# Kernel tuning notes

Hardware: AMD Instinct MI355X
Metric: run time of the kernel (lower is better)

The kernel has to match this reference:

```python
import jax, jax.numpy as jnp
import numpy as np

EPS = 1e-6


def setup_inputs() -> dict:
    key = jax.random.key(0)
    ks = jax.random.split(key, 7)
    T, B, D, n, r = 512, 32, 1024, 1024, 8
    x = jax.random.normal(ks[0], (T, B, D), dtype=jnp.float32)
    # xavier_uniform-like init for weights
    def xavier(k, shape):
        fan_in, fan_out = shape[1], shape[0]
        a = float(np.sqrt(6.0 / (fan_in + fan_out)))
        return jax.random.uniform(k, shape, dtype=jnp.float32, minval=-a, maxval=a)
    W_k = xavier(ks[1], (n, D))
    W_v = xavier(ks[2], (n, D))
    W_q = xavier(ks[3], (n, D))
    W_kr = xavier(ks[4], (r, n))
    U0 = jnp.zeros((B, n, r), dtype=jnp.float32)
    V0 = jax.random.normal(ks[5], (B, n, r), dtype=jnp.float32) * 0.01
    return {"x": x, "W_k": W_k, "W_v": W_v, "W_q": W_q, "W_kr": W_kr, "U0": U0, "V0": V0}


def reference(x, W_k, W_v, W_q, W_kr, U0, V0):
    # x: [T, B, D]; state S = U @ V^T with U,V: [B, n, r]
    k = jnp.einsum('tbd,nd->tbn', x, W_k)
    v = jnp.einsum('tbd,nd->tbn', x, W_v)
    q = jnp.einsum('tbd,nd->tbn', x, W_q)
    V = V0  # V is never updated in the recurrence

    def step(U, kvq):
        k_t, v_t, q_t = kvq  # each [B, n]
        k_norm = k_t / (jnp.linalg.norm(k_t, axis=-1, keepdims=True) + EPS)
        Vtk = jnp.einsum('bnr,bn->br', V, k_norm)
        retrieved = jnp.einsum('bnr,br->bn', U, Vtk)
        delta = v_t - retrieved
        k_r = k_norm @ W_kr.T  # [B, r]
        U_new = jnp.tanh(U + delta[:, :, None] * k_r[:, None, :])
        Vtq = jnp.einsum('bnr,bn->br', V, q_t)
        Sq = jnp.einsum('bnr,br->bn', U_new, Vtq)
        out = Sq * jax.nn.silu(Sq)
        return U_new, out

    U_final, output = jax.lax.scan(step, U0, (k, v, q))
    return output, (U_final, V)
```

## Files before the change

### kernel.cpp

```cpp
#include <hip/hip_runtime.h>
#include <hip/hip_bf16.h>

typedef __attribute__((ext_vector_type(8))) short short8;
typedef __attribute__((ext_vector_type(4))) short short4v;
typedef __attribute__((ext_vector_type(4))) float f32x4;
typedef unsigned short u16;

__device__ inline float b2f(u16 u) {
    unsigned int i = ((unsigned int)u) << 16;
    float f; __builtin_memcpy(&f, &i, 4); return f;
}
__device__ inline u16 f2b(float f) {
    unsigned int i; __builtin_memcpy(&i, &f, 4);
    unsigned int r = (i + 0x7FFFu + ((i >> 16) & 1u)) >> 16;
    return (u16)r;
}

__device__ inline float xsum32(float x) {
    unsigned u; __builtin_memcpy(&u, &x, 4);
    auto r = __builtin_amdgcn_permlane32_swap(u, u, false, false);
    unsigned s0 = r[0], s1 = r[1];
    float f0, f1; __builtin_memcpy(&f0, &s0, 4); __builtin_memcpy(&f1, &s1, 4);
    return f0 + f1;
}

#define GLDS(g, l) __builtin_amdgcn_global_load_lds( \
    (const __attribute__((address_space(1))) void*)(g), \
    (__attribute__((address_space(3))) void*)(l), 16, 0, 0)

#define KWAIT(N) asm volatile("s_waitcnt lgkmcnt(0)\n\t" \
                              "s_waitcnt vmcnt(" #N ")\n\t" \
                              "s_barrier" ::: "memory")

__global__ __launch_bounds__(256) void cvt_k(const float* __restrict__ src,
                                             u16* __restrict__ dst, int n4)
{
    const int i = blockIdx.x * blockDim.x + threadIdx.x;
    if (i < n4) {
        const f32x4 v = ((const f32x4*)src)[i];
        short4v o;
        o.x = (short)f2b(v.x); o.y = (short)f2b(v.y);
        o.z = (short)f2b(v.z); o.w = (short)f2b(v.w);
        ((short4v*)dst)[i] = o;
    }
}

__global__ __launch_bounds__(256) void vT_k(const float* __restrict__ V0,
                                            float* __restrict__ V0T)
{
    const int gid = blockIdx.x * 256 + threadIdx.x;
    const int b = gid >> 9, j = (gid >> 6) & 7, n0 = (gid & 63) * 16;
    const float* src = V0 + (long)b * 8192 + (long)n0 * 8 + j;
    float* dst = V0T + (long)b * 8192 + (long)j * 1024 + n0;
#pragma unroll
    for (int i = 0; i < 16; i += 4) {
        f32x4 o = { src[(i + 0) * 8], src[(i + 1) * 8],
                    src[(i + 2) * 8], src[(i + 3) * 8] };
        *(f32x4*)(dst + i) = o;
    }
}

__global__ __launch_bounds__(512) void gemm256_kvq(
    const u16* __restrict__ Xbf, const u16* __restrict__ Wbf,
    u16* __restrict__ Ko, u16* __restrict__ Vo, u16* __restrict__ Qo)
{
    __shared__ u16 lds[65536];

    const int bid = blockIdx.x;
    const int swz = (bid & 7) * 96 + (bid >> 3);
    const int bm = swz / 12, bnx = swz % 12;
    const int widx = bnx >> 2;
    const int nbase = (bnx & 3) * 256;
    const int m0 = bm * 256;
    const u16* Wp = Wbf + (long)widx * 1048576;
    u16* O = (widx == 0) ? Ko : (widx == 1 ? Vo : Qo);

    const int tid = threadIdx.x;
    const int w = tid >> 6;
    const int lane = tid & 63;
    const int wm = (w >> 2) * 128;
    const int wn = (w & 3) * 64;
    const int ln = lane & 15, qd = lane >> 4;

    const int q8 = lane >> 3, s8 = lane & 7;
    const int cc = s8 ^ q8;
    const u16* p0; const u16* p1; const u16* p2; const u16* p3;
    {
        auto mk = [&](int l) -> const u16* {
            const int r = l * 64 + w * 8 + q8;
            return (cc < 4)
                ? (Xbf + (long)(m0 + r) * 1024 + cc * 8)
                : (Wp  + (long)(nbase + r) * 1024 + (cc - 4) * 8);
        };
        p0 = mk(0); p1 = mk(1); p2 = mk(2); p3 = mk(3);
    }

    int aoff[8], boff[4];
#pragma unroll
    for (int mf = 0; mf < 8; ++mf) {
        const int ro = wm + mf * 16 + ln;
        aoff[mf] = ro * 128 + ((qd ^ (ro & 7)) * 16);
    }
#pragma unroll
    for (int nf = 0; nf < 4; ++nf) {
        const int rb = wn + nf * 16 + ln;
        boff[nf] = rb * 128 + (((4 + qd) ^ (rb & 7)) * 16);
    }

    f32x4 acc[8][4];
#pragma unroll
    for (int i = 0; i < 8; ++i)
#pragma unroll
        for (int j = 0; j < 4; ++j) acc[i][j] = (f32x4){0.f, 0.f, 0.f, 0.f};

#pragma unroll
    for (int tt = 0; tt < 3; ++tt) {
        char* db = (char*)lds + tt * 32768 + w * 1024;
        GLDS(p0, db);
        GLDS(p1, db + 8192);
        GLDS(p2, db + 16384);
        GLDS(p3, db + 24576);
        p0 += 32; p1 += 32; p2 += 32; p3 += 32;
    }
    KWAIT(8);

    for (int t = 0; t < 32; ++t) {
        const char* bb = (const char*)lds + (t & 3) * 32768;
        short8 a[8], bfr[4];
#pragma unroll
        for (int mf = 0; mf < 4; ++mf) a[mf] = *(const short8*)(bb + aoff[mf]);
#pragma unroll
        for (int nf = 0; nf < 4; ++nf) bfr[nf] = *(const short8*)(bb + boff[nf]);
        if (t < 29) {
            char* db = (char*)lds + ((t + 3) & 3) * 32768 + w * 1024;
            GLDS(p0, db);
            GLDS(p1, db + 8192);
            p0 += 32; p1 += 32;
        }
        __builtin_amdgcn_s_setprio(1);
#pragma unroll
        for (int mf = 0; mf < 4; ++mf)
#pragma unroll
            for (int nf = 0; nf < 4; ++nf)
                acc[mf][nf] = __builtin_amdgcn_mfma_f32_16x16x32_bf16(
                    a[mf], bfr[nf], acc[mf][nf], 0, 0, 0);
        __builtin_amdgcn_s_setprio(0);
#pragma unroll
        for (int mf = 4; mf < 8; ++mf) a[mf] = *(const short8*)(bb + aoff[mf]);
        if (t < 29) {
            char* db = (char*)lds + ((t + 3) & 3) * 32768 + w * 1024;
            GLDS(p2, db + 16384);
            GLDS(p3, db + 24576);
            p2 += 32; p3 += 32;
        }
        __builtin_amdgcn_s_setprio(1);
#pragma unroll
        for (int mf = 4; mf < 8; ++mf)
#pragma unroll
            for (int nf = 0; nf < 4; ++nf)
                acc[mf][nf] = __builtin_amdgcn_mfma_f32_16x16x32_bf16(
                    a[mf], bfr[nf], acc[mf][nf], 0, 0, 0);
        __builtin_amdgcn_s_setprio(0);
        if (t < 29)       KWAIT(8);
        else if (t == 29) KWAIT(4);
        else if (t == 30) KWAIT(0);
    }

#pragma unroll
    for (int mf = 0; mf < 8; ++mf) {
#pragma unroll
        for (int nf = 0; nf < 4; ++nf) {
            const int r0 = m0 + wm + mf * 16 + qd * 4;
            const int c  = nbase + wn + nf * 16 + ln;
#pragma unroll
            for (int r = 0; r < 4; ++r)
                O[(long)(r0 + r) * 1024 + c] = f2b(acc[mf][nf][r]);
        }
    }
}

__global__ __launch_bounds__(256) void scal_k(
    const u16* __restrict__ K, const u16* __restrict__ Q,
    const float* __restrict__ V0T, const float* __restrict__ Wkr,
    float* __restrict__ S)
{
    const int b  = blockIdx.x & 31;
    const int t0 = (blockIdx.x >> 5) * 4;
    const int tid = threadIdx.x;
    const int j = tid & 7, c = tid >> 3;
    const int n0 = c * 32;

    f32x4 vv[8], ww[8];
    {
        const f32x4* vp = (const f32x4*)(V0T + (long)b * 8192 + (long)j * 1024 + n0);
        const f32x4* wp = (const f32x4*)(Wkr + (long)j * 1024 + n0);
#pragma unroll
        for (int i = 0; i < 8; i++) { vv[i] = vp[i]; ww[i] = wp[i]; }
    }

    float avk[4], akr[4], avq[4], ass[4];
#pragma unroll
    for (int dt = 0; dt < 4; dt++) { avk[dt] = akr[dt] = avq[dt] = ass[dt] = 0.f; }

#pragma unroll
    for (int dt = 0; dt < 4; dt++) {
        const long m = (long)(t0 + dt) * 32 + b;
        const short8* kp = (const short8*)(K + m * 1024 + n0);
        const short8* qp = (const short8*)(Q + m * 1024 + n0);
#pragma unroll
        for (int i = 0; i < 4; i++) {
            const short8 kb = kp[i], qb = qp[i];
#pragma unroll
            for (int e = 0; e < 8; e++) {
                const int idx = i * 8 + e;
                const float kv = b2f((u16)kb[e]);
                const float qv = b2f((u16)qb[e]);
                const float vj = vv[idx >> 2][idx & 3];
                const float wj = ww[idx >> 2][idx & 3];
                avk[dt] = fmaf(vj, kv, avk[dt]);
                akr[dt] = fmaf(wj, kv, akr[dt]);
                avq[dt] = fmaf(vj, qv, avq[dt]);
                ass[dt] = fmaf(kv, kv, ass[dt]);
            }
        }
    }

    __shared__ float red[4][4][3][8];
    __shared__ float ssr[4][4];
    const int wave = tid >> 6, lane = tid & 63;
#pragma unroll
    for (int dt = 0; dt < 4; dt++) {
        float a = avk[dt], k2 = akr[dt], q = avq[dt], s = ass[dt];
#pragma unroll
        for (int off = 8; off < 64; off <<= 1) {
            a  += __shfl_xor(a,  off, 64);
            k2 += __shfl_xor(k2, off, 64);
            q  += __shfl_xor(q,  off, 64);
            s  += __shfl_xor(s,  off, 64);
        }
        if (lane < 8) {
            red[wave][dt][0][lane] = a;
            red[wave][dt][1][lane] = k2;
            red[wave][dt][2][lane] = q;
        }
        if (lane == 0) ssr[wave][dt] = s;
    }
    __syncthreads();
    if (tid < 128) {
        const int dt = tid >> 5, rr = tid & 31;
        if (rr < 24) {
            const int v = rr >> 3, jj = rr & 7;
            float s = red[0][dt][v][jj] + red[1][dt][v][jj] +
                      red[2][dt][v][jj] + red[3][dt][v][jj];
            if (v != 2) {
                const float n2 = ssr[0][dt] + ssr[1][dt] + ssr[2][dt] + ssr[3][dt];
                const float inv = 1.0f / (sqrtf(n2) + 1e-6f);
                s *= (v == 0) ? (0.5f * inv) : (2.0f * inv);
            } else {
                s *= 0.5f;
            }
            S[((long)b * 512 + t0 + dt) * 32 + v * 8 + jj] = s;
        }
    }
}

__global__ __launch_bounds__(128) void scan_k(
    const u16* __restrict__ Vbuf, const float* __restrict__ S,
    const float* __restrict__ U0, float* __restrict__ outp,
    float* __restrict__ Ufin)
{
    __shared__ float Sl[512 * 32];

    const int b = blockIdx.x >> 4;
    const int chunk = blockIdx.x & 15;
    const int wave = threadIdx.x >> 6, lane = threadIdx.x & 63;
    const int rh = lane >> 5;
    const int n = chunk * 64 + wave * 32 + (lane & 31);
    const int so = rh * 4;

    {
        const f32x4* Sg = (const f32x4*)(S + (long)b * 16384);
        f32x4* Sd = (f32x4*)Sl;
        for (int i = threadIdx.x; i < 4096; i += 128) Sd[i] = Sg[i];
    }

    float U[4];
    {
        const float* u0 = U0 + ((long)b * 1024 + n) * 8 + so;
#pragma unroll
        for (int j2 = 0; j2 < 4; j2++) U[j2] = 2.0f * u0[j2];
    }

    const u16* vp0 = Vbuf + (long)b * 1024 + n;
    u16 vnx[16];
#pragma unroll
    for (int i = 0; i < 16; i++) vnx[i] = vp0[(long)i * 32768];

    __syncthreads();

    f32x4 sc[3], sn[3];
#pragma unroll
    for (int r = 0; r < 3; r++) sc[r] = *(const f32x4*)&Sl[r * 8 + so];
#pragma unroll
    for (int r = 0; r < 3; r++) sn[r] = *(const f32x4*)&Sl[32 + r * 8 + so];

    float* op = outp + (long)b * 1024 + n;

    for (int t0 = 0; t0 < 512; t0 += 16) {
        float vcur[16];
#pragma unroll
        for (int i = 0; i < 16; i++) vcur[i] = b2f(vnx[i]);
        const int tn = (t0 + 16 < 512) ? (t0 + 16) : t0;
#pragma unroll
        for (int i = 0; i < 16; i++) vnx[i] = vp0[(long)(tn + i) * 32768];

#pragma unroll
        for (int i = 0; i < 16; i++) {
            const int t = t0 + i;
            const int tf = (t + 2 < 512) ? (t + 2) : t;
            f32x4 sm[3];
#pragma unroll
            for (int r = 0; r < 3; r++) sm[r] = *(const f32x4*)&Sl[tf * 32 + r * 8 + so];

            const f32x4 a = sc[0], Kk = sc[1], Qq = sc[2];
#pragma unroll
            for (int r = 0; r < 3; r++) { sc[r] = sn[r]; sn[r] = sm[r]; }

            float pr = fmaf(U[0], a.x, U[1] * a.y) + fmaf(U[2], a.z, U[3] * a.w);
            const float ret = xsum32(pr);
            const float delta = vcur[i] - ret;

            const float kr4[4] = {Kk.x, Kk.y, Kk.z, Kk.w};
            const float vq4[4] = {Qq.x, Qq.y, Qq.z, Qq.w};

            float sq0 = 0.f, sq1 = 0.f;
#pragma unroll
            for (int j2 = 0; j2 < 4; j2++) {
                const float xx = fmaf(delta, kr4[j2], U[j2]);
                const float e = __expf(xx);
                const float rc = __builtin_amdgcn_rcpf(e + 1.0f);
                const float u = fmaf(-4.0f, rc, 2.0f);
                U[j2] = u;
                if (j2 & 1) sq1 = fmaf(u, vq4[j2], sq1);
                else        sq0 = fmaf(u, vq4[j2], sq0);
            }
            const float Sq = xsum32(sq0 + sq1);
            const float sg = __builtin_amdgcn_rcpf(1.0f + __expf(-Sq));
            const float o = Sq * Sq * sg;
            if (rh == 0) op[(long)t * 32768] = o;
        }
    }

    *(f32x4*)(Ufin + ((long)b * 1024 + n) * 8 + so) =
        (f32x4){0.5f * U[0], 0.5f * U[1], 0.5f * U[2], 0.5f * U[3]};
}

__global__ __launch_bounds__(256) void vcopy_k(const float* __restrict__ src,
                                               float* __restrict__ dst)
{
    const int i = blockIdx.x * blockDim.x + threadIdx.x;
    ((f32x4*)dst)[i] = ((const f32x4*)src)[i];
}

extern "C" void kernel_launch(void* const* d_in, const int* in_sizes, int n_in,
                              void* d_out, int out_size, void* d_ws, size_t ws_size,
                              hipStream_t stream)
{
    const float* x   = (const float*)d_in[0];
    const float* Wk  = (const float*)d_in[1];
    const float* Wv  = (const float*)d_in[2];
    const float* Wq  = (const float*)d_in[3];
    const float* Wkr = (const float*)d_in[4];
    const float* U0  = (const float*)d_in[5];
    const float* V0  = (const float*)d_in[6];
    float* out = (float*)d_out;

    char* ws = (char*)d_ws;
    u16*   Xbf = (u16*)(ws);
    u16*   Wbf = (u16*)(ws + 33554432);
    u16*   Kb  = (u16*)(ws + 39845888);
    u16*   Vb  = (u16*)(ws + 73400320);
    u16*   Qb  = (u16*)(ws + 106954752);
    float* Sc  = (float*)(ws + 140509184);
    float* V0T = (float*)(ws + 142606336);

    cvt_k<<<16384, 256, 0, stream>>>(x,  Xbf,               4194304);
    cvt_k<<<1024,  256, 0, stream>>>(Wk, Wbf,                262144);
    cvt_k<<<1024,  256, 0, stream>>>(Wv, Wbf + 1048576,      262144);
    cvt_k<<<1024,  256, 0, stream>>>(Wq, Wbf + 2097152,      262144);
    vT_k <<<64,    256, 0, stream>>>(V0, V0T);

    gemm256_kvq<<<768, 512, 0, stream>>>(Xbf, Wbf, Kb, Vb, Qb);
    scal_k  <<<4096, 256, 0, stream>>>(Kb, Qb, V0T, Wkr, Sc);
    scan_k  <<<512, 128, 0, stream>>>(Vb, Sc, U0, out, out + 16777216);
    vcopy_k <<<256, 256, 0, stream>>>(V0, out + 17039360);
}
```

Baseline: 409.2 us.

## Fold V0^T·W_q into per-batch projection to skip the Q GEMM

Since V never changes, V^T q_t = (V0^T W_q) x_t. A small kernel precomputes Aq = V0^T W_q per batch (B×r×D), so scal_k dots x directly against Aq. This drops the full Q projection GEMM (a third of the big GEMM) and the Q conversion and storage. The scan kernel also swaps the rotating two-step LDS prefetch for a 4-slot ring buffer loaded after the U update. The cost is an extra fp32 fold kernel and bf16 x feeding the Q path in place of bf16 q, which slightly changes rounding.

Result: slower. 506.8 us (+23.9%).

```diff
diff --git a/kernel.cpp b/kernel.cpp
--- a/kernel.cpp
+++ b/kernel.cpp
@@ -60,20 +60,49 @@
     }
 }
 
-__global__ __launch_bounds__(512) void gemm256_kvq(
+__global__ __launch_bounds__(256) void foldq_k(const float* __restrict__ V0T,
+                                               const float* __restrict__ Wq,
+                                               float* __restrict__ Aq)
+{
+    const int rb = blockIdx.x >> 3, dc = blockIdx.x & 7;
+    const int dl = threadIdx.x & 127, g = threadIdx.x >> 7;
+    const int d = dc * 128 + dl;
+    __shared__ float rs[8][1024];
+    {
+        float* rf = (float*)rs;
+        const float* sp = V0T + (long)rb * 8192;
+        for (int i = threadIdx.x; i < 8192; i += 256) rf[i] = sp[i];
+    }
+    __syncthreads();
+    float acc[4] = {0.f, 0.f, 0.f, 0.f};
+    const float* wp = Wq + d;
+#pragma unroll 4
+    for (int n = 0; n < 1024; ++n) {
+        const float w = wp[(long)n * 1024];
+        acc[0] = fmaf(rs[g * 4 + 0][n], w, acc[0]);
+        acc[1] = fmaf(rs[g * 4 + 1][n], w, acc[1]);
+        acc[2] = fmaf(rs[g * 4 + 2][n], w, acc[2]);
+        acc[3] = fmaf(rs[g * 4 + 3][n], w, acc[3]);
+    }
+#pragma unroll
+    for (int r = 0; r < 4; ++r)
+        Aq[(long)(rb * 8 + g * 4 + r) * 1024 + d] = acc[r];
+}
+
+__global__ __launch_bounds__(512) void gemm256_kv(
     const u16* __restrict__ Xbf, const u16* __restrict__ Wbf,
-    u16* __restrict__ Ko, u16* __restrict__ Vo, u16* __restrict__ Qo)
+    u16* __restrict__ Ko, u16* __restrict__ Vo)
 {
     __shared__ u16 lds[65536];
 
     const int bid = blockIdx.x;
-    const int swz = (bid & 7) * 96 + (bid >> 3);
-    const int bm = swz / 12, bnx = swz % 12;
+    const int swz = (bid & 7) * 64 + (bid >> 3);
+    const int bm = swz >> 3, bnx = swz & 7;
     const int widx = bnx >> 2;
     const int nbase = (bnx & 3) * 256;
     const int m0 = bm * 256;
     const u16* Wp = Wbf + (long)widx * 1048576;
-    u16* O = (widx == 0) ? Ko : (widx == 1 ? Vo : Qo);
+    u16* O = (widx == 0) ? Ko : Vo;
 
     const int tid = threadIdx.x;
     const int w = tid >> 6;
@@ -180,9 +209,9 @@
 }
 
 __global__ __launch_bounds__(256) void scal_k(
-    const u16* __restrict__ K, const u16* __restrict__ Q,
+    const u16* __restrict__ K, const u16* __restrict__ X,
     const float* __restrict__ V0T, const float* __restrict__ Wkr,
-    float* __restrict__ S)
+    const float* __restrict__ Aq, float* __restrict__ S)
 {
     const int b  = blockIdx.x & 31;
     const int t0 = (blockIdx.x >> 5) * 4;
@@ -190,12 +219,13 @@
     const int j = tid & 7, c = tid >> 3;
     const int n0 = c * 32;
 
-    f32x4 vv[8], ww[8];
+    f32x4 vv[8], ww[8], aqv[8];
     {
         const f32x4* vp = (const f32x4*)(V0T + (long)b * 8192 + (long)j * 1024 + n0);
         const f32x4* wp = (const f32x4*)(Wkr + (long)j * 1024 + n0);
-#pragma unroll
-        for (int i = 0; i < 8; i++) { vv[i] = vp[i]; ww[i] = wp[i]; }
+        const f32x4* ap = (const f32x4*)(Aq + (long)(b * 8 + j) * 1024 + n0);
+#pragma unroll
+        for (int i = 0; i < 8; i++) { vv[i] = vp[i]; ww[i] = wp[i]; aqv[i] = ap[i]; }
     }
 
     float avk[4], akr[4], avq[4], ass[4];
@@ -206,20 +236,21 @@
     for (int dt = 0; dt < 4; dt++) {
         const long m = (long)(t0 + dt) * 32 + b;
         const short8* kp = (const short8*)(K + m * 1024 + n0);
-        const short8* qp = (const short8*)(Q + m * 1024 + n0);
+        const short8* xp = (const short8*)(X + m * 1024 + n0);
 #pragma unroll
         for (int i = 0; i < 4; i++) {
-            const short8 kb = kp[i], qb = qp[i];
+            const short8 kb = kp[i], xb = xp[i];
 #pragma unroll
             for (int e = 0; e < 8; e++) {
                 const int idx = i * 8 + e;
                 const float kv = b2f((u16)kb[e]);
-                const float qv = b2f((u16)qb[e]);
+                const float xv = b2f((u16)xb[e]);
                 const float vj = vv[idx >> 2][idx & 3];
                 const float wj = ww[idx >> 2][idx & 3];
+                const float aj = aqv[idx >> 2][idx & 3];
                 avk[dt] = fmaf(vj, kv, avk[dt]);
                 akr[dt] = fmaf(wj, kv, akr[dt]);
-                avq[dt] = fmaf(vj, qv, avq[dt]);
+                avq[dt] = fmaf(aj, xv, avq[dt]);
                 ass[dt] = fmaf(kv, kv, ass[dt]);
             }
         }
@@ -298,11 +329,12 @@
 
     __syncthreads();
 
-    f32x4 sc[3], sn[3];
-#pragma unroll
-    for (int r = 0; r < 3; r++) sc[r] = *(const f32x4*)&Sl[r * 8 + so];
-#pragma unroll
-    for (int r = 0; r < 3; r++) sn[r] = *(const f32x4*)&Sl[32 + r * 8 + so];
+    f32x4 sb[4][3];
+#pragma unroll
+    for (int s = 0; s < 4; ++s)
+#pragma unroll
+        for (int r = 0; r < 3; ++r)
+            sb[s][r] = *(const f32x4*)&Sl[s * 32 + r * 8 + so];
 
     float* op = outp + (long)b * 1024 + n;
 
@@ -317,14 +349,8 @@
 #pragma unroll
         for (int i = 0; i < 16; i++) {
             const int t = t0 + i;
-            const int tf = (t + 2 < 512) ? (t + 2) : t;
-            f32x4 sm[3];
-#pragma unroll
-            for (int r = 0; r < 3; r++) sm[r] = *(const f32x4*)&Sl[tf * 32 + r * 8 + so];
-
-            const f32x4 a = sc[0], Kk = sc[1], Qq = sc[2];
-#pragma unroll
-            for (int r = 0; r < 3; r++) { sc[r] = sn[r]; sn[r] = sm[r]; }
+            const int slot = i & 3;
+            const f32x4 a = sb[slot][0], Kk = sb[slot][1], Qq = sb[slot][2];
 
             float pr = fmaf(U[0], a.x, U[1] * a.y) + fmaf(U[2], a.z, U[3] * a.w);
             const float ret = xsum32(pr);
@@ -344,6 +370,12 @@
                 if (j2 & 1) sq1 = fmaf(u, vq4[j2], sq1);
                 else        sq0 = fmaf(u, vq4[j2], sq0);
             }
+
+            const int tf = (t + 4 < 512) ? (t + 4) : 511;
+#pragma unroll
+            for (int r = 0; r < 3; r++)
+                sb[slot][r] = *(const f32x4*)&Sl[tf * 32 + r * 8 + so];
+
             const float Sq = xsum32(sq0 + sq1);
             const float sg = __builtin_amdgcn_rcpf(1.0f + __expf(-Sq));
             const float o = Sq * Sq * sg;
@@ -380,18 +412,18 @@
     u16*   Wbf = (u16*)(ws + 33554432);
     u16*   Kb  = (u16*)(ws + 39845888);
     u16*   Vb  = (u16*)(ws + 73400320);
-    u16*   Qb  = (u16*)(ws + 106954752);
+    float* Aq  = (float*)(ws + 106954752);
     float* Sc  = (float*)(ws + 140509184);
     float* V0T = (float*)(ws + 142606336);
 
     cvt_k<<<16384, 256, 0, stream>>>(x,  Xbf,               4194304);
     cvt_k<<<1024,  256, 0, stream>>>(Wk, Wbf,                262144);
     cvt_k<<<1024,  256, 0, stream>>>(Wv, Wbf + 1048576,      262144);
-    cvt_k<<<1024,  256, 0, stream>>>(Wq, Wbf + 2097152,      262144);
     vT_k <<<64,    256, 0, stream>>>(V0, V0T);
-
-    gemm256_kvq<<<768, 512, 0, stream>>>(Xbf, Wbf, Kb, Vb, Qb);
-    scal_k  <<<4096, 256, 0, stream>>>(Kb, Qb, V0T, Wkr, Sc);
+    foldq_k<<<256, 256, 0, stream>>>(V0T, Wq, Aq);
+
+    gemm256_kv<<<512, 512, 0, stream>>>(Xbf, Wbf, Kb, Vb);
+    scal_k  <<<4096, 256, 0, stream>>>(Kb, Xbf, V0T, Wkr, Aq, Sc);
     scan_k  <<<512, 128, 0, stream>>>(Vb, Sc, U0, out, out + 16777216);
     vcopy_k <<<256, 256, 0, stream>>>(V0, out + 17039360);
 }
```
